# Performance work log

Hardware: AMD Instinct MI355X
Metric: run time of the kernel (lower is better)

The kernel has to match this reference:

```python
import jax, jax.numpy as jnp
import numpy as np

N = 50000; E = 1600000; H = 128; R = 8; T = 2; P = 1000; M = 223


def setup_inputs() -> dict:
    key = jax.random.key(0)
    ks = jax.random.split(key, 16)
    s = 1.0 / np.sqrt(H).astype(np.float32)
    inp = {}
    inp['neigh_type_count'] = jax.random.uniform(ks[0], (N, 2), dtype=jnp.float32) * 5.0
    inp['norm'] = jax.random.uniform(ks[1], (E,), dtype=jnp.float32) + 0.1
    inp['special_cost'] = jax.random.uniform(ks[2], (N,), dtype=jnp.float32)
    inp['gt_map'] = jax.random.uniform(ks[3], (M, M), dtype=jnp.float32)
    inp['fc_w'] = jax.random.normal(ks[4], (2, H), dtype=jnp.float32) * (1.0 / np.sqrt(2.0))
    inp['fc_b'] = jnp.zeros((H,), jnp.float32)
    inp['w_nt'] = jax.random.normal(ks[5], (T, H, H), dtype=jnp.float32) * s
    inp['w_rel'] = jax.random.normal(ks[6], (R, H, H), dtype=jnp.float32) * s
    inp['fc2_w'] = jax.random.normal(ks[7], (H, 1), dtype=jnp.float32) * s
    inp['fc2_b'] = jnp.zeros((1,), jnp.float32)
    inp['fc3_w'] = jax.random.normal(ks[8], (H, 1), dtype=jnp.float32) * s
    inp['fc3_b'] = jnp.zeros((1,), jnp.float32)
    inp['fl3_w'] = jax.random.normal(ks[9], (H, P), dtype=jnp.float32) * s
    inp['fl3_b'] = jnp.zeros((P,), jnp.float32)
    inp['node_type'] = jax.random.randint(ks[10], (N,), 0, T, dtype=jnp.int32)
    inp['src'] = jax.random.randint(ks[11], (E,), 0, N, dtype=jnp.int32)
    inp['dst'] = jax.random.randint(ks[12], (E,), 0, N, dtype=jnp.int32)
    inp['etype'] = jax.random.randint(ks[13], (E,), 0, R, dtype=jnp.int32)
    return inp


def reference(neigh_type_count, norm, special_cost, gt_map, fc_w, fc_b, w_nt, w_rel,
              fc2_w, fc2_b, fc3_w, fc3_b, fl3_w, fl3_b, node_type, src, dst, etype):
    n = neigh_type_count.shape[0]
    # fc: [N,2] -> [N,H]
    h0 = neigh_type_count @ fc_w + fc_b
    # input RGCN layer: per-src-node-type transform, then per-edge-relation transform.
    # Compute node x type / node x relation products once, then gather per edge
    # (same math as per-edge bmm with gathered weights, far less traffic).
    h_nt_all = jnp.einsum('ni,tio->nto', h0, w_nt)                 # [N,T,H]
    h_nt = jnp.take_along_axis(h_nt_all, node_type[:, None, None].astype(jnp.int32), axis=1)[:, 0, :]  # [N,H]
    h_rel = jnp.einsum('ni,rio->nro', h_nt, w_rel)                 # [N,R,H]
    msg = h_rel[src, etype] * norm[:, None]                        # [E,H]
    h = jax.ops.segment_sum(msg, dst, num_segments=n)              # scatter-sum -> [N,H]
    h = jax.nn.relu(h)                                             # apply_func activation
    # fc2 + clamp(sigmoid)
    pred = jnp.clip(jax.nn.sigmoid(h @ fc2_w + fc2_b), 1e-7, 1e10) # [N,1]
    m = gt_map.shape[0]
    pm = pred[:m * m, 0].reshape(m, m)                             # pred node map [M,M]
    ce = -jnp.sum(gt_map * jnp.log2(pm))                           # min cross-entropy (single GT map)
    rs = jnp.sum(pm, axis=1)                                       # row sums [M]
    cs = jnp.sum(pm, axis=0)                                       # col sums [M]
    loss2 = jnp.sum(pm * (rs[:, None] - pm)) + jnp.sum(pm * (cs[None, :] - pm))
    sumone = jnp.sum((rs - 1.0) ** 2) + jnp.sum((cs - 1.0) ** 2)
    # fc_for_loss3 (sigmoid probs; summed so params get grads)
    prob3_sum = jnp.sum(jax.nn.sigmoid(h @ fl3_w + fl3_b))
    # OutputLayer: scatter-sum src pred_prob to dst, (sum-1)^2 * special_cost
    agg = jax.ops.segment_sum(pred[src, 0], dst, num_segments=n)
    out_cost = jnp.sum(((agg - 1.0) ** 2) * special_cost)
    # dgl.mean_nodes (single graph) + fc3
    gembed = jnp.mean(h, axis=0)
    pred_obj = (gembed @ fc3_w + fc3_b)[0]
    return jnp.stack([pred_obj, sumone, loss2, ce, out_cost, prob3_sum])
```

## Files before the change

kernel.cpp:

```cpp
#include <hip/hip_runtime.h>

#define H 128
#define RNUM 8
#define TNUM 2
#define PNUM 1000
#define MNUM 223
#define BNODES 64
#define NBUCK 782
#define BCAP 2304
#define EPB 8192
#define CPAD 16

typedef __attribute__((ext_vector_type(8))) short bf16x8;
typedef __attribute__((ext_vector_type(4))) float f32x4;

__device__ __forceinline__ float fsig(float z) {
    return 1.0f / (1.0f + __expf(-z));
}
__device__ __forceinline__ float fsig_fast(float z) {
    return __builtin_amdgcn_rcpf(1.0f + __expf(-z));
}

__device__ __forceinline__ float wave_reduce(float v) {
#pragma unroll
    for (int off = 32; off > 0; off >>= 1) v += __shfl_down(v, off, 64);
    return v;
}

__device__ __forceinline__ unsigned short f2bf(float f) {
    unsigned int u = __float_as_uint(f);
    u += 0x7fffu + ((u >> 16) & 1u);
    return (unsigned short)(u >> 16);
}

__global__ __launch_bounds__(1024) void partition_setup(
        const int* __restrict__ src, const int* __restrict__ dst,
        const int* __restrict__ etype, const float* __restrict__ norm,
        const int* __restrict__ node_type, const float* __restrict__ ntc,
        int* __restrict__ cursor,
        uint2* __restrict__ buck, int E, int NP,
        const float* __restrict__ fl3_w, const float* __restrict__ fl3_b,
        unsigned short* __restrict__ wt, float* __restrict__ biasws,
        const float* __restrict__ fc_w, const float* __restrict__ fc_b,
        const float* __restrict__ w_nt, const float* __restrict__ w_rel,
        unsigned short* __restrict__ CbT) {
    int blk = blockIdx.x;
    int tid = threadIdx.x;
    if (blk < NP) {
        __shared__ int lh[NBUCK];
        __shared__ int gb[NBUCK];
        for (int i = tid; i < NBUCK; i += 1024) lh[i] = 0;
        __syncthreads();
        int base = blk * EPB;
        int e0 = base + tid * 8;
        int s[8], d[8], r[8]; float nm[8];
        if (e0 + 8 <= E) {
            *(int4*)(s)      = ((const int4*)(src + e0))[0];
            *(int4*)(s + 4)  = ((const int4*)(src + e0))[1];
            *(int4*)(d)      = ((const int4*)(dst + e0))[0];
            *(int4*)(d + 4)  = ((const int4*)(dst + e0))[1];
            *(int4*)(r)      = ((const int4*)(etype + e0))[0];
            *(int4*)(r + 4)  = ((const int4*)(etype + e0))[1];
            *(float4*)(nm)     = ((const float4*)(norm + e0))[0];
            *(float4*)(nm + 4) = ((const float4*)(norm + e0))[1];
        } else {
#pragma unroll
            for (int c = 0; c < 8; ++c) {
                int e = e0 + c;
                bool ok = (e < E);
                s[c] = ok ? src[e] : 0;
                d[c] = ok ? dst[e] : 0;
                r[c] = ok ? etype[e] : 0;
                nm[c] = ok ? norm[e] : 0.0f;
            }
        }
        int t8[8]; float2 cc8[8];
#pragma unroll
        for (int c = 0; c < 8; ++c) {
            t8[c] = node_type[s[c]];
            cc8[c] = ((const float2*)ntc)[s[c]];
        }
        uint2 pl[8]; int bb[8]; int rk[8];
#pragma unroll
        for (int c = 0; c < 8; ++c) {
            bb[c] = -1;
            if (e0 + c < E) {
                unsigned f0 = __float2uint_rn(nm[c] * cc8[c].x * 128.0f);
                unsigned f1 = __float2uint_rn(nm[c] * cc8[c].y * 128.0f);
                unsigned f2 = __float2uint_rn(nm[c] * 512.0f);
                int b = d[c] >> 6;
                int local = d[c] & 63;
                pl[c].x = (unsigned)s[c] | ((unsigned)local << 18) | ((unsigned)r[c] << 24) | ((unsigned)t8[c] << 27);
                pl[c].y = f0 | (f1 << 10) | (f2 << 20);
                bb[c] = b;
                rk[c] = atomicAdd(&lh[b], 1);
            }
        }
        __syncthreads();
        for (int i = tid; i < NBUCK; i += 1024) {
            if (lh[i] > 0) {
                int g = atomicAdd(&cursor[i * CPAD], lh[i]);
                gb[i] = (g < 0) ? 0 : (g > BCAP ? BCAP : g);
            }
        }
        __syncthreads();
#pragma unroll
        for (int c = 0; c < 8; ++c) {
            if (bb[c] >= 0) {
                int pos = gb[bb[c]] + rk[c];
                if (pos < BCAP) buck[(size_t)bb[c] * BCAP + pos] = pl[c];
            }
        }
    } else if (blk < NP + 128) {
        int p = (blk - NP) * 8 + (tid >> 7);
        int k = tid & 127;
        float v = (p < PNUM) ? fl3_w[(size_t)k * PNUM + p] : 0.0f;
        wt[(size_t)p * H + k] = f2bf(v);
        if (k == 0) biasws[p] = (p < PNUM) ? fl3_b[p] : -1.0e4f;
    } else {
        __shared__ float G[8][3][H];
        int g = tid >> 7;
        int tr = (blk - NP - 128) * 8 + g;
        int t = tr >> 3, r = tr & 7;
        int i = tid & 127;
        float a0 = 0.f, a1 = 0.f, a2 = 0.f;
#pragma unroll 8
        for (int j = 0; j < H; ++j) {
            float w = w_nt[((size_t)t * H + j) * H + i];
            a0 += fc_w[j] * w;
            a1 += fc_w[H + j] * w;
            a2 += fc_b[j] * w;
        }
        G[g][0][i] = a0; G[g][1][i] = a1; G[g][2][i] = a2;
        __syncthreads();
        float c0 = 0.f, c1 = 0.f, c2 = 0.f;
#pragma unroll 8
        for (int k = 0; k < H; ++k) {
            float w = w_rel[((size_t)r * H + k) * H + i];
            c0 += G[g][0][k] * w;
            c1 += G[g][1][k] * w;
            c2 += G[g][2][k] * w;
        }
        CbT[i * 64 + tr * 3 + 0] = f2bf(c0);
        CbT[i * 64 + tr * 3 + 1] = f2bf(c1);
        CbT[i * 64 + tr * 3 + 2] = f2bf(c2);
        if (tr == 0) {
            uint4 z = make_uint4(0u, 0u, 0u, 0u);
            *(uint4*)(CbT + i * 64 + 48) = z;
            *(uint4*)(CbT + i * 64 + 56) = z;
        }
    }
}

__global__ __launch_bounds__(256) void bucket_node(
        const uint2* __restrict__ buck, const int* __restrict__ cursor,
        const unsigned short* __restrict__ CbT,
        const float* __restrict__ fc2_w, const float* __restrict__ fc2_b,
        unsigned short* __restrict__ hb, float* __restrict__ pred,
        float* __restrict__ gpart, int N) {
    __shared__ float S[64 * 68];
    __shared__ float gloc[128];
    unsigned long long* P = (unsigned long long*)S;
    unsigned short* hsh = (unsigned short*)S;
    int tid = threadIdx.x;
    int bkt = blockIdx.x;
    int lane = tid & 63, w = tid >> 6;
    int lrow = lane & 15, quad = lane >> 4;

    for (int i = tid; i < 2048; i += 256) S[i] = 0.0f;
    if (tid < 128) gloc[tid] = 0.0f;
    __syncthreads();

    int cnt = cursor[bkt * CPAD];
    if (cnt > BCAP) cnt = BCAP;
    if (cnt < 0) cnt = 0;
    const uint2* bp = buck + (size_t)bkt * BCAP;
    for (int base = 0; base < cnt; base += 2048) {
        uint2 pl[8]; int ii[8];
#pragma unroll
        for (int j = 0; j < 8; ++j) {
            ii[j] = base + j * 256 + tid;
            pl[j] = (ii[j] < cnt) ? bp[ii[j]] : make_uint2(0u, 0u);
        }
#pragma unroll
        for (int j = 0; j < 8; ++j) {
            if (ii[j] < cnt) {
                int local = (pl[j].x >> 18) & 63;
                int tr = (pl[j].x >> 24) & 15;
                unsigned y = pl[j].y;
                unsigned long long pk = (unsigned long long)(y & 1023u)
                                      | ((unsigned long long)((y >> 10) & 1023u) << 21)
                                      | ((unsigned long long)(y >> 20) << 42);
                atomicAdd(&P[local * 16 + tr], pk);
            }
        }
    }
    __syncthreads();

    unsigned long long rpk[4];
#pragma unroll
    for (int u = 0; u < 4; ++u) rpk[u] = P[tid * 4 + u];
    __syncthreads();
#pragma unroll
    for (int u = 0; u < 4; ++u) {
        int idx = tid * 4 + u;
        int local = idx >> 4, tr = idx & 15;
        float* p = S + local * 68 + tr * 3;
        p[0] = (float)(unsigned)(rpk[u] & 0x1FFFFFull) * (1.0f / 128.0f);
        p[1] = (float)(unsigned)((rpk[u] >> 21) & 0x1FFFFFull) * (1.0f / 128.0f);
        p[2] = (float)(unsigned)(rpk[u] >> 42) * (1.0f / 512.0f);
    }
    for (int idx = tid; idx < 1024; idx += 256) {
        int row = idx >> 4, c = idx & 15;
        S[row * 68 + 48 + c] = 0.0f;
    }
    __syncthreads();

    bf16x8 a[2];
#pragma unroll
    for (int ks = 0; ks < 2; ++ks) {
        const float* sp = S + (w * 16 + lrow) * 68 + ks * 32 + quad * 8;
        float4 f0 = *(const float4*)sp;
        float4 f1 = *(const float4*)(sp + 4);
        bf16x8 t;
        t[0] = (short)f2bf(f0.x); t[1] = (short)f2bf(f0.y);
        t[2] = (short)f2bf(f0.z); t[3] = (short)f2bf(f0.w);
        t[4] = (short)f2bf(f1.x); t[5] = (short)f2bf(f1.y);
        t[6] = (short)f2bf(f1.z); t[7] = (short)f2bf(f1.w);
        a[ks] = t;
    }
    __syncthreads();

    f32x4 acc[8];
#pragma unroll
    for (int tn = 0; tn < 8; ++tn) acc[tn] = (f32x4){0.f, 0.f, 0.f, 0.f};
#pragma unroll
    for (int ks = 0; ks < 2; ++ks) {
#pragma unroll
        for (int tn = 0; tn < 8; ++tn) {
            bf16x8 b = *(const bf16x8*)(CbT + (size_t)(tn * 16 + lrow) * 64 + ks * 32 + quad * 8);
            acc[tn] = __builtin_amdgcn_mfma_f32_16x16x32_bf16(a[ks], b, acc[tn], 0, 0, 0);
        }
    }
#pragma unroll
    for (int tn = 0; tn < 8; ++tn)
#pragma unroll
        for (int r = 0; r < 4; ++r) acc[tn][r] = fmaxf(acc[tn][r], 0.f);

#pragma unroll
    for (int r = 0; r < 4; ++r) {
        unsigned short* hrow = hsh + (w * 16 + quad * 4 + r) * 136 + lrow;
#pragma unroll
        for (int tn = 0; tn < 8; ++tn) hrow[tn * 16] = f2bf(acc[tn][r]);
    }
    int vbase = bkt * BNODES + w * 16 + quad * 4;
    float pd[4];
#pragma unroll
    for (int r = 0; r < 4; ++r) {
        float s = 0.f;
#pragma unroll
        for (int tn = 0; tn < 8; ++tn) s += acc[tn][r] * fc2_w[tn * 16 + lrow];
        pd[r] = s;
    }
#pragma unroll
    for (int mask = 1; mask < 16; mask <<= 1)
#pragma unroll
        for (int r = 0; r < 4; ++r) pd[r] += __shfl_xor(pd[r], mask, 64);
    if (lrow == 0) {
#pragma unroll
        for (int r = 0; r < 4; ++r) {
            int v = vbase + r;
            if (v < N) {
                float z = pd[r] + fc2_b[0];
                pred[v] = fminf(fmaxf(fsig(z), 1e-7f), 1e10f);
            }
        }
    }
    float csum[8];
#pragma unroll
    for (int tn = 0; tn < 8; ++tn)
        csum[tn] = acc[tn][0] + acc[tn][1] + acc[tn][2] + acc[tn][3];
#pragma unroll
    for (int mask = 16; mask < 64; mask <<= 1)
#pragma unroll
        for (int tn = 0; tn < 8; ++tn) csum[tn] += __shfl_xor(csum[tn], mask, 64);
    if (lane < 16) {
#pragma unroll
        for (int tn = 0; tn < 8; ++tn) atomicAdd(&gloc[tn * 16 + lrow], csum[tn]);
    }
    __syncthreads();
    if (tid < 128) gpart[(size_t)bkt * 128 + tid] = gloc[tid];

#pragma unroll
    for (int i = 0; i < 4; ++i) {
        int row = i * 16 + (tid >> 4);
        int cc = tid & 15;
        uint4 v = *(const uint4*)(hsh + row * 136 + cc * 8);
        *(uint4*)(hb + (size_t)(bkt * BNODES + row) * H + cc * 8) = v;
    }
}

__global__ __launch_bounds__(256, 2) void mega_kernel(
        const unsigned short* __restrict__ hb, const unsigned short* __restrict__ wt,
        const float* __restrict__ biasws, float* __restrict__ psum, int nb128,
        const uint2* __restrict__ buck, const int* __restrict__ cursor,
        const float* __restrict__ pred, const float* __restrict__ sc,
        const float* __restrict__ gt, float* __restrict__ ocpart, int N,
        float* __restrict__ rs, float* __restrict__ cs,
        float* __restrict__ cepart, float* __restrict__ sqpart,
        const float* __restrict__ gpart, float* __restrict__ gsum, int nbuck) {
    __shared__ unsigned short Bsh[128 * 136];
    __shared__ float red[12];
    int blk = blockIdx.x;
    int tid = threadIdx.x;
    int P1 = nb128;
    int P2 = P1 + nbuck;
    int P3 = P2 + 2 * MNUM;

    if (blk < P1) {
        int n0 = blk * 128;
        int lane = tid & 63, wid = tid >> 6;
        int wy = wid >> 1, wx = wid & 1;
        int lrow = lane & 15, quad = lane >> 4;

        bf16x8 a[4][4];
#pragma unroll
        for (int tm = 0; tm < 4; ++tm) {
            const unsigned short* arow = hb + (size_t)(n0 + wy * 64 + tm * 16 + lrow) * H + quad * 8;
#pragma unroll
            for (int ks = 0; ks < 4; ++ks)
                a[tm][ks] = *(const bf16x8*)(arow + ks * 32);
        }

        float lsum = 0.f;
        for (int pt = 0; pt < 8; ++pt) {
            __syncthreads();
            {
                int c = tid & 15;
                int r0 = tid >> 4;
#pragma unroll
                for (int it = 0; it < 8; ++it) {
                    int row = r0 + it * 16;
                    uint4 bv = *(const uint4*)(wt + (size_t)(pt * 128 + row) * H + c * 8);
                    *(uint4*)(Bsh + row * 136 + c * 8) = bv;
                }
            }
            __syncthreads();

            f32x4 acc[4][4];
#pragma unroll
            for (int tm = 0; tm < 4; ++tm)
#pragma unroll
                for (int tn = 0; tn < 4; ++tn)
                    acc[tm][tn] = (f32x4){0.f, 0.f, 0.f, 0.f};

            const unsigned short* Bbase = Bsh + (wx * 64 + lrow) * 136 + quad * 8;
#pragma unroll
            for (int ks = 0; ks < 4; ++ks) {
                bf16x8 b[4];
#pragma unroll
                for (int tn = 0; tn < 4; ++tn)
                    b[tn] = *(const bf16x8*)(Bbase + tn * 16 * 136 + ks * 32);
#pragma unroll
                for (int tm = 0; tm < 4; ++tm)
#pragma unroll
                    for (int tn = 0; tn < 4; ++tn)
                        acc[tm][tn] = __builtin_amdgcn_mfma_f32_16x16x32_bf16(a[tm][ks], b[tn], acc[tm][tn], 0, 0, 0);
            }

#pragma unroll
            for (int tn = 0; tn < 4; ++tn) {
                float bv = biasws[pt * 128 + wx * 64 + tn * 16 + lrow];
#pragma unroll
                for (int tm = 0; tm < 4; ++tm) {
#pragma unroll
                    for (int r = 0; r < 4; ++r)
                        lsum += fsig_fast(acc[tm][tn][r] + bv);
                }
            }
        }
        lsum = wave_reduce(lsum);
        if (lane == 0) red[wid] = lsum;
        __syncthreads();
        if (tid == 0)
            psum[blk] = red[0] + red[1] + red[2] + red[3];
    } else if (blk < P2) {
        int bkt = blk - P1;
        float* agg = (float*)Bsh;
        if (tid < BNODES) agg[tid] = 0.0f;
        __syncthreads();
        int cnt = cursor[bkt * CPAD];
        if (cnt > BCAP) cnt = BCAP;
        if (cnt < 0) cnt = 0;
        const uint2* bp = buck + (size_t)bkt * BCAP;
        for (int base = 0; base < cnt; base += 2048) {
            unsigned x[8]; float pv[8]; int ii[8];
#pragma unroll
            for (int j = 0; j < 8; ++j) {
                ii[j] = base + j * 256 + tid;
                x[j] = (ii[j] < cnt) ? bp[ii[j]].x : 0u;
            }
#pragma unroll
            for (int j = 0; j < 8; ++j)
                pv[j] = (ii[j] < cnt) ? pred[x[j] & 0x3FFFF] : 0.f;
#pragma unroll
            for (int j = 0; j < 8; ++j)
                if (ii[j] < cnt) atomicAdd(&agg[(x[j] >> 18) & 63], pv[j]);
        }
        __syncthreads();
        if (tid < 64) {
            float v = 0.f;
            int node = bkt * BNODES + tid;
            if (node < N) {
                float d = agg[tid] - 1.0f;
                v = d * d * sc[node];
            }
            v = wave_reduce(v);
            if (tid == 0) ocpart[bkt] = v;
        }
    } else if (blk < P3) {
        int rc = blk - P2;
        if (rc < MNUM) {
            float p = 0.f, ce = 0.f, sq = 0.f;
            if (tid < MNUM) {
                p = pred[rc * MNUM + tid];
                ce = -gt[rc * MNUM + tid] * __log2f(p);
                sq = p * p;
            }
            p = wave_reduce(p);
            ce = wave_reduce(ce);
            sq = wave_reduce(sq);
            int wid = tid >> 6;
            if ((tid & 63) == 0) { red[wid] = p; red[4 + wid] = ce; red[8 + wid] = sq; }
            __syncthreads();
            if (tid == 0) {
                rs[rc] = red[0] + red[1] + red[2] + red[3];
                cepart[rc] = red[4] + red[5] + red[6] + red[7];
                sqpart[rc] = red[8] + red[9] + red[10] + red[11];
            }
        } else {
            int j = rc - MNUM;
            float p = 0.f;
            if (tid < MNUM) p = pred[tid * MNUM + j];
            p = wave_reduce(p);
            if ((tid & 63) == 0) red[tid >> 6] = p;
            __syncthreads();
            if (tid == 0) cs[j] = red[0] + red[1] + red[2] + red[3];
        }
    } else {
        int dim = blk - P3;
        float s = 0.f;
        for (int b = tid; b < nbuck; b += 256) s += gpart[(size_t)b * 128 + dim];
        s = wave_reduce(s);
        if ((tid & 63) == 0) red[tid >> 6] = s;
        __syncthreads();
        if (tid == 0) gsum[dim] = red[0] + red[1] + red[2] + red[3];
    }
}

__global__ __launch_bounds__(1024) void tail_kernel(
        const float* __restrict__ rs, const float* __restrict__ cs,
        const float* __restrict__ cepart, const float* __restrict__ sqpart,
        const float* __restrict__ psum, int npsum,
        const float* __restrict__ ocpart, int nbuck,
        const float* __restrict__ gsum, const float* __restrict__ fc3_w,
        const float* __restrict__ fc3_b, const float* __restrict__ fl3_b,
        float* __restrict__ out, int N, int padrows) {
    __shared__ float red[16];
    int tid = threadIdx.x;
    int wid = tid >> 6, lane = tid & 63;
    float v = 0.f;
    if (tid < MNUM) {
        float a = rs[tid] - 1.0f, b = cs[tid] - 1.0f;
        v = a * a + b * b;
    }
    v = wave_reduce(v);
    if (lane == 0) red[wid] = v;
    __syncthreads();
    if (tid == 0) { float s = 0.f; for (int i = 0; i < 16; ++i) s += red[i]; out[1] = s; }
    __syncthreads();
    float ce = (tid < MNUM) ? cepart[tid] : 0.f;
    ce = wave_reduce(ce);
    if (lane == 0) red[wid] = ce;
    __syncthreads();
    if (tid == 0) { float s = 0.f; for (int i = 0; i < 16; ++i) s += red[i]; out[3] = s; }
    __syncthreads();
    float l2 = 0.f;
    if (tid < MNUM)
        l2 = rs[tid] * rs[tid] + cs[tid] * cs[tid] - 2.0f * sqpart[tid];
    l2 = wave_reduce(l2);
    if (lane == 0) red[wid] = l2;
    __syncthreads();
    if (tid == 0) { float s = 0.f; for (int i = 0; i < 16; ++i) s += red[i]; out[2] = s; }
    __syncthreads();
    float ps = 0.f;
    for (int i = tid; i < npsum; i += 1024) ps += psum[i];
    float ss = 0.f;
    for (int p = tid; p < PNUM; p += 1024) ss += fsig_fast(fl3_b[p]);
    float comb = ps - (float)padrows * ss;
    comb = wave_reduce(comb);
    if (lane == 0) red[wid] = comb;
    __syncthreads();
    if (tid == 0) { float s = 0.f; for (int i = 0; i < 16; ++i) s += red[i]; out[5] = s; }
    __syncthreads();
    float oc = 0.f;
    for (int b = tid; b < nbuck; b += 1024) oc += ocpart[b];
    oc = wave_reduce(oc);
    if (lane == 0) red[wid] = oc;
    __syncthreads();
    if (tid == 0) { float s = 0.f; for (int i = 0; i < 16; ++i) s += red[i]; out[4] = s; }
    __syncthreads();
    float pv = 0.f;
    if (tid < 128) pv = gsum[tid] * (1.0f / (float)N) * fc3_w[tid];
    pv = wave_reduce(pv);
    if (lane == 0) red[wid] = pv;
    __syncthreads();
    if (tid == 0) { float s = 0.f; for (int i = 0; i < 16; ++i) s += red[i]; out[0] = s + fc3_b[0]; }
}

extern "C" void kernel_launch(void* const* d_in, const int* in_sizes, int n_in,
                              void* d_out, int out_size, void* d_ws, size_t ws_size,
                              hipStream_t stream) {
    const float* ntc   = (const float*)d_in[0];
    const float* norm  = (const float*)d_in[1];
    const float* sc    = (const float*)d_in[2];
    const float* gt    = (const float*)d_in[3];
    const float* fc_w  = (const float*)d_in[4];
    const float* fc_b  = (const float*)d_in[5];
    const float* w_nt  = (const float*)d_in[6];
    const float* w_rel = (const float*)d_in[7];
    const float* fc2_w = (const float*)d_in[8];
    const float* fc2_b = (const float*)d_in[9];
    const float* fc3_w = (const float*)d_in[10];
    const float* fc3_b = (const float*)d_in[11];
    const float* fl3_w = (const float*)d_in[12];
    const float* fl3_b = (const float*)d_in[13];
    const int* node_type = (const int*)d_in[14];
    const int* src   = (const int*)d_in[15];
    const int* dst   = (const int*)d_in[16];
    const int* etype = (const int*)d_in[17];
    int N = in_sizes[2];
    int E = in_sizes[1];
    int nb128 = (N + 127) / 128;
    int padN  = nb128 * 128;
    int nbuck = padN / BNODES;
    int npsum = nb128;
    int NP = (E + EPB - 1) / EPB;

    float* ws   = (float*)d_ws;
    unsigned short* wt = (unsigned short*)ws;
    float* biasws = ws + 65536;
    float* gsum = ws + 66560;
    float* rs   = ws + 66688;
    float* cs   = ws + 66944;
    int*  cursor = (int*)(ws + 67200);
    float* psum = ws + 79744;
    float* cepart = ws + 80768;
    float* sqpart = ws + 81024;
    float* ocpart = ws + 81280;
    unsigned short* CbT = (unsigned short*)(ws + 82304);
    float* gpart  = ws + 86400;
    float* pred = ws + 186496;
    unsigned short* hb = (unsigned short*)(ws + 236496);
    uint2* buck = (uint2*)(ws + 3439568);
    float* out  = (float*)d_out;

    hipMemsetAsync(cursor, 0, NBUCK * CPAD * sizeof(int), stream);

    partition_setup<<<NP + 130, 1024, 0, stream>>>(src, dst, etype, norm, node_type, ntc,
                                                   cursor, buck, E, NP,
                                                   fl3_w, fl3_b, wt, biasws,
                                                   fc_w, fc_b, w_nt, w_rel, CbT);
    bucket_node<<<nbuck, 256, 0, stream>>>(buck, cursor, CbT, fc2_w, fc2_b,
                                           hb, pred, gpart, N);
    int megablocks = nb128 + nbuck + 2 * MNUM + 128;
    mega_kernel<<<megablocks, 256, 0, stream>>>(hb, wt, biasws, psum, nb128,
                                                buck, cursor, pred, sc, gt, ocpart, N,
                                                rs, cs, cepart, sqpart, gpart, gsum, nbuck);
    tail_kernel<<<1, 1024, 0, stream>>>(rs, cs, cepart, sqpart, psum, npsum, ocpart, nbuck,
                                        gsum, fc3_w, fc3_b, fl3_b, out, N, padN - N);
}
```

Baseline: 192.7 us.

## Split edge bucket payload into SoA arrays and fold tail into mega kernel

Bucket payload storage moves from interleaved uint2 to two separate 32-bit arrays. The mega kernel's scatter phase only reads the x component, so it now fetches half the bytes. The separate single-block tail kernel is removed: the last mega_kernel block to finish, detected with an atomic counter and thread fences, performs the final reductions. This saves one launch but adds an atomic and fences to every block, and the tail reductions now run with 256 threads instead of 1024.

New measurement: 321.4 us. 66.7% more time.

```diff
diff --git a/kernel.cpp b/kernel.cpp
--- a/kernel.cpp
+++ b/kernel.cpp
@@ -38,7 +38,7 @@
         const int* __restrict__ etype, const float* __restrict__ norm,
         const int* __restrict__ node_type, const float* __restrict__ ntc,
         int* __restrict__ cursor,
-        uint2* __restrict__ buck, int E, int NP,
+        unsigned* __restrict__ bx, unsigned* __restrict__ by, int E, int NP,
         const float* __restrict__ fl3_w, const float* __restrict__ fl3_b,
         unsigned short* __restrict__ wt, float* __restrict__ biasws,
         const float* __restrict__ fc_w, const float* __restrict__ fc_b,
@@ -80,7 +80,7 @@
             t8[c] = node_type[s[c]];
             cc8[c] = ((const float2*)ntc)[s[c]];
         }
-        uint2 pl[8]; int bb[8]; int rk[8];
+        unsigned px[8], py[8]; int bb[8]; int rk[8];
 #pragma unroll
         for (int c = 0; c < 8; ++c) {
             bb[c] = -1;
@@ -90,8 +90,8 @@
                 unsigned f2 = __float2uint_rn(nm[c] * 512.0f);
                 int b = d[c] >> 6;
                 int local = d[c] & 63;
-                pl[c].x = (unsigned)s[c] | ((unsigned)local << 18) | ((unsigned)r[c] << 24) | ((unsigned)t8[c] << 27);
-                pl[c].y = f0 | (f1 << 10) | (f2 << 20);
+                px[c] = (unsigned)s[c] | ((unsigned)local << 18) | ((unsigned)r[c] << 24) | ((unsigned)t8[c] << 27);
+                py[c] = f0 | (f1 << 10) | (f2 << 20);
                 bb[c] = b;
                 rk[c] = atomicAdd(&lh[b], 1);
             }
@@ -108,7 +108,11 @@
         for (int c = 0; c < 8; ++c) {
             if (bb[c] >= 0) {
                 int pos = gb[bb[c]] + rk[c];
-                if (pos < BCAP) buck[(size_t)bb[c] * BCAP + pos] = pl[c];
+                if (pos < BCAP) {
+                    size_t off = (size_t)bb[c] * BCAP + pos;
+                    bx[off] = px[c];
+                    by[off] = py[c];
+                }
             }
         }
     } else if (blk < NP + 128) {
@@ -153,7 +157,8 @@
 }
 
 __global__ __launch_bounds__(256) void bucket_node(
-        const uint2* __restrict__ buck, const int* __restrict__ cursor,
+        const unsigned* __restrict__ bx, const unsigned* __restrict__ by,
+        const int* __restrict__ cursor,
         const unsigned short* __restrict__ CbT,
         const float* __restrict__ fc2_w, const float* __restrict__ fc2_b,
         unsigned short* __restrict__ hb, float* __restrict__ pred,
@@ -174,20 +179,24 @@
     int cnt = cursor[bkt * CPAD];
     if (cnt > BCAP) cnt = BCAP;
     if (cnt < 0) cnt = 0;
-    const uint2* bp = buck + (size_t)bkt * BCAP;
+    const unsigned* bpx = bx + (size_t)bkt * BCAP;
+    const unsigned* bpy = by + (size_t)bkt * BCAP;
     for (int base = 0; base < cnt; base += 2048) {
-        uint2 pl[8]; int ii[8];
+        unsigned x8[8], y8[8]; int ii[8];
 #pragma unroll
         for (int j = 0; j < 8; ++j) {
             ii[j] = base + j * 256 + tid;
-            pl[j] = (ii[j] < cnt) ? bp[ii[j]] : make_uint2(0u, 0u);
-        }
+            x8[j] = (ii[j] < cnt) ? bpx[ii[j]] : 0u;
+        }
+#pragma unroll
+        for (int j = 0; j < 8; ++j)
+            y8[j] = (ii[j] < cnt) ? bpy[ii[j]] : 0u;
 #pragma unroll
         for (int j = 0; j < 8; ++j) {
             if (ii[j] < cnt) {
-                int local = (pl[j].x >> 18) & 63;
-                int tr = (pl[j].x >> 24) & 15;
-                unsigned y = pl[j].y;
+                int local = (x8[j] >> 18) & 63;
+                int tr = (x8[j] >> 24) & 15;
+                unsigned y = y8[j];
                 unsigned long long pk = (unsigned long long)(y & 1023u)
                                       | ((unsigned long long)((y >> 10) & 1023u) << 21)
                                       | ((unsigned long long)(y >> 20) << 42);
@@ -303,23 +312,27 @@
 __global__ __launch_bounds__(256, 2) void mega_kernel(
         const unsigned short* __restrict__ hb, const unsigned short* __restrict__ wt,
         const float* __restrict__ biasws, float* __restrict__ psum, int nb128,
-        const uint2* __restrict__ buck, const int* __restrict__ cursor,
+        const unsigned* __restrict__ bx, const int* __restrict__ cursor,
         const float* __restrict__ pred, const float* __restrict__ sc,
         const float* __restrict__ gt, float* __restrict__ ocpart, int N,
         float* __restrict__ rs, float* __restrict__ cs,
         float* __restrict__ cepart, float* __restrict__ sqpart,
-        const float* __restrict__ gpart, float* __restrict__ gsum, int nbuck) {
+        const float* __restrict__ gpart, float* __restrict__ gsum, int nbuck,
+        int* __restrict__ done, int totblocks,
+        const float* __restrict__ fc3_w, const float* __restrict__ fc3_b,
+        const float* __restrict__ fl3_b, float* __restrict__ out, int padrows) {
     __shared__ unsigned short Bsh[128 * 136];
     __shared__ float red[12];
+    __shared__ int isLast;
     int blk = blockIdx.x;
     int tid = threadIdx.x;
+    int lane = tid & 63, wid = tid >> 6;
     int P1 = nb128;
     int P2 = P1 + nbuck;
     int P3 = P2 + 2 * MNUM;
 
     if (blk < P1) {
         int n0 = blk * 128;
-        int lane = tid & 63, wid = tid >> 6;
         int wy = wid >> 1, wx = wid & 1;
         int lrow = lane & 15, quad = lane >> 4;
 
@@ -392,13 +405,13 @@
         int cnt = cursor[bkt * CPAD];
         if (cnt > BCAP) cnt = BCAP;
         if (cnt < 0) cnt = 0;
-        const uint2* bp = buck + (size_t)bkt * BCAP;
+        const unsigned* bp = bx + (size_t)bkt * BCAP;
         for (int base = 0; base < cnt; base += 2048) {
             unsigned x[8]; float pv[8]; int ii[8];
 #pragma unroll
             for (int j = 0; j < 8; ++j) {
                 ii[j] = base + j * 256 + tid;
-                x[j] = (ii[j] < cnt) ? bp[ii[j]].x : 0u;
+                x[j] = (ii[j] < cnt) ? bp[ii[j]] : 0u;
             }
 #pragma unroll
             for (int j = 0; j < 8; ++j)
@@ -430,8 +443,7 @@
             p = wave_reduce(p);
             ce = wave_reduce(ce);
             sq = wave_reduce(sq);
-            int wid = tid >> 6;
-            if ((tid & 63) == 0) { red[wid] = p; red[4 + wid] = ce; red[8 + wid] = sq; }
+            if (lane == 0) { red[wid] = p; red[4 + wid] = ce; red[8 + wid] = sq; }
             __syncthreads();
             if (tid == 0) {
                 rs[rc] = red[0] + red[1] + red[2] + red[3];
@@ -443,7 +455,7 @@
             float p = 0.f;
             if (tid < MNUM) p = pred[tid * MNUM + j];
             p = wave_reduce(p);
-            if ((tid & 63) == 0) red[tid >> 6] = p;
+            if (lane == 0) red[wid] = p;
             __syncthreads();
             if (tid == 0) cs[j] = red[0] + red[1] + red[2] + red[3];
         }
@@ -452,38 +464,36 @@
         float s = 0.f;
         for (int b = tid; b < nbuck; b += 256) s += gpart[(size_t)b * 128 + dim];
         s = wave_reduce(s);
-        if ((tid & 63) == 0) red[tid >> 6] = s;
+        if (lane == 0) red[wid] = s;
         __syncthreads();
         if (tid == 0) gsum[dim] = red[0] + red[1] + red[2] + red[3];
     }
-}
-
-__global__ __launch_bounds__(1024) void tail_kernel(
-        const float* __restrict__ rs, const float* __restrict__ cs,
-        const float* __restrict__ cepart, const float* __restrict__ sqpart,
-        const float* __restrict__ psum, int npsum,
-        const float* __restrict__ ocpart, int nbuck,
-        const float* __restrict__ gsum, const float* __restrict__ fc3_w,
-        const float* __restrict__ fc3_b, const float* __restrict__ fl3_b,
-        float* __restrict__ out, int N, int padrows) {
-    __shared__ float red[16];
-    int tid = threadIdx.x;
-    int wid = tid >> 6, lane = tid & 63;
+
+    __threadfence();
+    if (tid == 0) {
+        int v = atomicAdd(done, 1);
+        isLast = (v == totblocks - 1) ? 1 : 0;
+    }
+    __syncthreads();
+    if (!isLast) return;
+    __threadfence();
+    __syncthreads();
+
     float v = 0.f;
     if (tid < MNUM) {
-        float a = rs[tid] - 1.0f, b = cs[tid] - 1.0f;
-        v = a * a + b * b;
+        float a_ = rs[tid] - 1.0f, b_ = cs[tid] - 1.0f;
+        v = a_ * a_ + b_ * b_;
     }
     v = wave_reduce(v);
     if (lane == 0) red[wid] = v;
     __syncthreads();
-    if (tid == 0) { float s = 0.f; for (int i = 0; i < 16; ++i) s += red[i]; out[1] = s; }
+    if (tid == 0) out[1] = red[0] + red[1] + red[2] + red[3];
     __syncthreads();
     float ce = (tid < MNUM) ? cepart[tid] : 0.f;
     ce = wave_reduce(ce);
     if (lane == 0) red[wid] = ce;
     __syncthreads();
-    if (tid == 0) { float s = 0.f; for (int i = 0; i < 16; ++i) s += red[i]; out[3] = s; }
+    if (tid == 0) out[3] = red[0] + red[1] + red[2] + red[3];
     __syncthreads();
     float l2 = 0.f;
     if (tid < MNUM)
@@ -491,31 +501,31 @@
     l2 = wave_reduce(l2);
     if (lane == 0) red[wid] = l2;
     __syncthreads();
-    if (tid == 0) { float s = 0.f; for (int i = 0; i < 16; ++i) s += red[i]; out[2] = s; }
+    if (tid == 0) out[2] = red[0] + red[1] + red[2] + red[3];
     __syncthreads();
     float ps = 0.f;
-    for (int i = tid; i < npsum; i += 1024) ps += psum[i];
+    for (int i = tid; i < nb128; i += 256) ps += psum[i];
     float ss = 0.f;
-    for (int p = tid; p < PNUM; p += 1024) ss += fsig_fast(fl3_b[p]);
+    for (int p = tid; p < PNUM; p += 256) ss += fsig_fast(fl3_b[p]);
     float comb = ps - (float)padrows * ss;
     comb = wave_reduce(comb);
     if (lane == 0) red[wid] = comb;
     __syncthreads();
-    if (tid == 0) { float s = 0.f; for (int i = 0; i < 16; ++i) s += red[i]; out[5] = s; }
+    if (tid == 0) out[5] = red[0] + red[1] + red[2] + red[3];
     __syncthreads();
     float oc = 0.f;
-    for (int b = tid; b < nbuck; b += 1024) oc += ocpart[b];
+    for (int b = tid; b < nbuck; b += 256) oc += ocpart[b];
     oc = wave_reduce(oc);
     if (lane == 0) red[wid] = oc;
     __syncthreads();
-    if (tid == 0) { float s = 0.f; for (int i = 0; i < 16; ++i) s += red[i]; out[4] = s; }
+    if (tid == 0) out[4] = red[0] + red[1] + red[2] + red[3];
     __syncthreads();
     float pv = 0.f;
     if (tid < 128) pv = gsum[tid] * (1.0f / (float)N) * fc3_w[tid];
     pv = wave_reduce(pv);
     if (lane == 0) red[wid] = pv;
     __syncthreads();
-    if (tid == 0) { float s = 0.f; for (int i = 0; i < 16; ++i) s += red[i]; out[0] = s + fc3_b[0]; }
+    if (tid == 0) out[0] = red[0] + red[1] + fc3_b[0];
 }
 
 extern "C" void kernel_launch(void* const* d_in, const int* in_sizes, int n_in,
@@ -544,7 +554,6 @@
     int nb128 = (N + 127) / 128;
     int padN  = nb128 * 128;
     int nbuck = padN / BNODES;
-    int npsum = nb128;
     int NP = (E + EPB - 1) / EPB;
 
     float* ws   = (float*)d_ws;
@@ -554,29 +563,31 @@
     float* rs   = ws + 66688;
     float* cs   = ws + 66944;
     int*  cursor = (int*)(ws + 67200);
-    float* psum = ws + 79744;
-    float* cepart = ws + 80768;
-    float* sqpart = ws + 81024;
-    float* ocpart = ws + 81280;
-    unsigned short* CbT = (unsigned short*)(ws + 82304);
-    float* gpart  = ws + 86400;
-    float* pred = ws + 186496;
-    unsigned short* hb = (unsigned short*)(ws + 236496);
-    uint2* buck = (uint2*)(ws + 3439568);
+    int*  done   = (int*)(ws + 79712);
+    float* psum = ws + 79760;
+    float* cepart = ws + 80784;
+    float* sqpart = ws + 81040;
+    float* ocpart = ws + 81296;
+    unsigned short* CbT = (unsigned short*)(ws + 82320);
+    float* gpart  = ws + 86416;
+    float* pred = ws + 186512;
+    unsigned short* hb = (unsigned short*)(ws + 236512);
+    unsigned* bx = (unsigned*)(ws + 3439584);
+    unsigned* by = (unsigned*)(ws + 5241312);
     float* out  = (float*)d_out;
 
-    hipMemsetAsync(cursor, 0, NBUCK * CPAD * sizeof(int), stream);
+    hipMemsetAsync(cursor, 0, (NBUCK * CPAD + CPAD) * sizeof(int), stream);
 
     partition_setup<<<NP + 130, 1024, 0, stream>>>(src, dst, etype, norm, node_type, ntc,
-                                                   cursor, buck, E, NP,
+                                                   cursor, bx, by, E, NP,
                                                    fl3_w, fl3_b, wt, biasws,
                                                    fc_w, fc_b, w_nt, w_rel, CbT);
-    bucket_node<<<nbuck, 256, 0, stream>>>(buck, cursor, CbT, fc2_w, fc2_b,
+    bucket_node<<<nbuck, 256, 0, stream>>>(bx, by, cursor, CbT, fc2_w, fc2_b,
                                            hb, pred, gpart, N);
     int megablocks = nb128 + nbuck + 2 * MNUM + 128;
     mega_kernel<<<megablocks, 256, 0, stream>>>(hb, wt, biasws, psum, nb128,
-                                                buck, cursor, pred, sc, gt, ocpart, N,
-                                                rs, cs, cepart, sqpart, gpart, gsum, nbuck);
-    tail_kernel<<<1, 1024, 0, stream>>>(rs, cs, cepart, sqpart, psum, npsum, ocpart, nbuck,
-                                        gsum, fc3_w, fc3_b, fl3_b, out, N, padN - N);
-}
+                                                bx, cursor, pred, sc, gt, ocpart, N,
+                                                rs, cs, cepart, sqpart, gpart, gsum, nbuck,
+                                                done, megablocks,
+                                                fc3_w, fc3_b, fl3_b, out, padN - N);
+}
```
